# Kernel optimization log

Hardware: AMD Instinct MI355X
Metric: run time of the kernel (lower is better)

The kernel has to match this reference:

```python
import jax, jax.numpy as jnp
import numpy as np

B, N, K = 4, 4096, 16
D_POINTS, D_MODEL = 64, 128


def setup_inputs() -> dict:
    key = jax.random.key(0)
    ks = jax.random.split(key, 18)
    rn = lambda k, shp, s=0.05: (jax.random.normal(k, shp, jnp.float32) * s)
    return {
        "xyz": jax.random.normal(ks[0], (B, N, 3), jnp.float32),
        "features": jax.random.normal(ks[1], (B, N, D_POINTS), jnp.float32),
        # fc_delta: Linear(3,d_model) -> ReLU -> Linear(d_model,d_model)
        "Wd1": rn(ks[2], (3, D_MODEL)), "bd1": rn(ks[3], (D_MODEL,)),
        "Wd2": rn(ks[4], (D_MODEL, D_MODEL)), "bd2": rn(ks[5], (D_MODEL,)),
        # fc1: Linear(d_points, d_model)
        "Wf1": rn(ks[6], (D_POINTS, D_MODEL)), "bf1": rn(ks[7], (D_MODEL,)),
        # w_qs / w_ks / w_vs: Linear(d_model, d_model, bias=False)
        "Wq": rn(ks[8], (D_MODEL, D_MODEL)),
        "Wk": rn(ks[9], (D_MODEL, D_MODEL)),
        "Wv": rn(ks[10], (D_MODEL, D_MODEL)),
        # fc_gamma: Linear(d_model,d_model) -> ReLU -> Linear(d_model,d_model)
        "Wg1": rn(ks[11], (D_MODEL, D_MODEL)), "bg1": rn(ks[12], (D_MODEL,)),
        "Wg2": rn(ks[13], (D_MODEL, D_MODEL)), "bg2": rn(ks[14], (D_MODEL,)),
        # fc2: Linear(d_model, d_points)
        "Wo": rn(ks[15], (D_MODEL, D_POINTS)), "bo": rn(ks[16], (D_POINTS,)),
    }


def reference(xyz, features, Wd1, bd1, Wd2, bd2, Wf1, bf1, Wq, Wk, Wv,
              Wg1, bg1, Wg2, bg2, Wo, bo):
    sq = jnp.sum(xyz * xyz, axis=-1)
    d2 = sq[:, :, None] + sq[:, None, :] - 2.0 * jnp.einsum('bnd,bmd->bnm', xyz, xyz)
    # argsort()[:, :, :k] == k smallest distances (self included)
    _, knn_idx = jax.lax.top_k(-d2, K)  # [B,N,K] int32

    gather = jax.vmap(lambda a, i: a[i])  # per-batch fancy gather along point axis
    knn_xyz = gather(xyz, knn_idx)                       # [B,N,K,3]
    rel = xyz[:, :, None, :] - knn_xyz                   # [B,N,K,3]
    pos_enc = jax.nn.relu(rel @ Wd1 + bd1) @ Wd2 + bd2   # [B,N,K,D]

    shortcut = features
    f = features @ Wf1 + bf1                             # [B,N,D]
    knn_f = gather(f, knn_idx)                           # [B,N,K,D]

    q = f @ Wq                                           # [B,N,D]
    k = knn_f @ Wk                                       # [B,N,K,D]
    v = knn_f @ Wv                                       # [B,N,K,D]

    attn = q[:, :, None, :] - k + pos_enc                # [B,N,K,D]
    attn = jax.nn.relu(attn @ Wg1 + bg1) @ Wg2 + bg2
    attn = jax.nn.softmax(attn / np.sqrt(D_MODEL).astype(np.float32), axis=-2)

    res = jnp.einsum('bnkf,bnkf->bnf', attn, v + pos_enc)  # [B,N,D]
    return res @ Wo + bo + shortcut                        # [B,N,d_points]
```

## Files before the change

kernel.cpp:

```cpp
#include <hip/hip_runtime.h>
#include <hip/hip_bf16.h>

#define NPTS 4096
#define BATCH 4
#define BN (BATCH * NPTS)
#define DMODEL 128
#define DPTS 64
#define KNBR 16
#define SWS 136

typedef unsigned short u16;
typedef unsigned int u32;
typedef unsigned long long u64;
typedef short bh8 __attribute__((ext_vector_type(8)));
typedef float f32x4 __attribute__((ext_vector_type(4)));

__device__ __forceinline__ float bfu(u16 u) {
    union { u32 i; float f; } c; c.i = ((u32)u) << 16; return c.f;
}
__device__ __forceinline__ u16 f2u(float x) {
    u32 u = __float_as_uint(x);
    u32 r = u + 0x7FFFu + ((u >> 16) & 1u);
    return (u16)(r >> 16);
}
__device__ __forceinline__ u32 pack2(float a, float b) {
    return (u32)f2u(a) | ((u32)f2u(b) << 16);
}
__device__ __forceinline__ float ldr(const void* p, long i, int mode) {
    return mode == 0 ? bfu(((const u16*)p)[i]) : ((const float*)p)[i];
}
__device__ __forceinline__ void str(void* p, long i, float v, int mode) {
    if (mode == 0) ((u16*)p)[i] = f2u(v);
    else ((float*)p)[i] = v;
}
__device__ __forceinline__ int detect_mode(const void* Wq) {
    const u16* w = (const u16*)Wq;
    int lane = threadIdx.x & 63;
    int tot = 0;
#pragma unroll
    for (int r = 0; r < 4; ++r) {
        unsigned e = (w[lane + r * 64] >> 7) & 0xFFu;
        bool wild = (e >= 132u) || (e > 0u && e <= 90u);
        tot += (int)__popcll(__ballot(wild));
    }
    return tot > 32 ? 1 : 0;
}

__global__ __launch_bounds__(256) void prep_kernel(
    const void* __restrict__ Wd2, const void* __restrict__ Wg1, const void* __restrict__ Wg2,
    const void* __restrict__ Wo, const void* __restrict__ Wq, const void* __restrict__ Wk,
    const void* __restrict__ Wv, const void* __restrict__ Wf1,
    u16* __restrict__ WdT2, u16* __restrict__ WgT1, u16* __restrict__ WgT2,
    u16* __restrict__ WoT, u16* __restrict__ WqT, u16* __restrict__ WkT,
    u16* __restrict__ WvT, u16* __restrict__ WfT) {
    int mode = detect_mode(Wq);
    int gid = blockIdx.x * 256 + threadIdx.x;
    if (gid < 6 * 16384) {
        int m = gid >> 14, o = gid & 16383;
        int n = o >> 7, i = o & 127;
        const void* W = (m == 0) ? Wd2 : (m == 1) ? Wg1 : (m == 2) ? Wg2
                      : (m == 3) ? Wq  : (m == 4) ? Wk  : Wv;
        u16* D = (m == 0) ? WdT2 : (m == 1) ? WgT1 : (m == 2) ? WgT2
               : (m == 3) ? WqT  : (m == 4) ? WkT  : WvT;
        D[o] = f2u(ldr(W, (long)i * 128 + n, mode));
    } else if (gid < 6 * 16384 + 8192) {
        int o = gid - 6 * 16384;
        int n = o >> 6, k2 = o & 63;
        WfT[o] = f2u(ldr(Wf1, (long)k2 * 128 + n, mode));
    } else if (gid < 6 * 16384 + 16384) {
        int o2 = gid - 6 * 16384 - 8192;
        int col = o2 >> 7, i = o2 & 127;
        WoT[o2] = f2u(ldr(Wo, (long)i * 64 + col, mode));
    }
}

__global__ __launch_bounds__(256) void qkv_kernel(
    const void* __restrict__ feat, const void* __restrict__ bf1v, const void* __restrict__ WqRaw,
    const u16* __restrict__ WfT, const u16* __restrict__ WqT,
    const u16* __restrict__ WkT, const u16* __restrict__ WvT,
    u16* __restrict__ qw, u16* __restrict__ kfw, u16* __restrict__ vfw) {
    int mode = detect_mode(WqRaw);
    __shared__ __align__(16) u16 sFeat[64 * 72];
    __shared__ __align__(16) u16 sF[64 * SWS];
    const int t = threadIdx.x;
    const int p0 = blockIdx.x * 64;
    const int lane = t & 63, w = t >> 6;
    const int rg = (w & 1) * 32, cg = (w >> 1) * 64;
    const int lm = lane & 15, lq = lane >> 4;

    for (int i = t; i < 512; i += 256) {
        int r = i >> 3, c8 = i & 7;
        u16 tmp[8];
        if (mode == 0) {
            *(uint4*)tmp = *((const uint4*)feat + (long)(p0 + r) * 8 + c8);
        } else {
            const float* fp = (const float*)feat + (long)(p0 + r) * 64 + c8 * 8;
#pragma unroll
            for (int u = 0; u < 8; ++u) tmp[u] = f2u(fp[u]);
        }
        *(uint4*)(sFeat + r * 72 + c8 * 8) = *(uint4*)tmp;
    }
    __syncthreads();

    {
        f32x4 acc[2][4];
#pragma unroll
        for (int rt = 0; rt < 2; ++rt)
#pragma unroll
            for (int ct = 0; ct < 4; ++ct) { acc[rt][ct][0]=0.f; acc[rt][ct][1]=0.f; acc[rt][ct][2]=0.f; acc[rt][ct][3]=0.f; }
#pragma unroll
        for (int kk = 0; kk < 2; ++kk) {
            const int ko = kk * 32 + lq * 8;
            bh8 a0 = *(const bh8*)(sFeat + (rg + lm) * 72 + ko);
            bh8 a1 = *(const bh8*)(sFeat + (rg + 16 + lm) * 72 + ko);
            bh8 bq[4];
#pragma unroll
            for (int ct = 0; ct < 4; ++ct)
                bq[ct] = *(const bh8*)(WfT + (long)(cg + ct * 16 + lm) * 64 + ko);
#pragma unroll
            for (int ct = 0; ct < 4; ++ct) {
                acc[0][ct] = __builtin_amdgcn_mfma_f32_16x16x32_bf16(a0, bq[ct], acc[0][ct], 0, 0, 0);
                acc[1][ct] = __builtin_amdgcn_mfma_f32_16x16x32_bf16(a1, bq[ct], acc[1][ct], 0, 0, 0);
            }
        }
#pragma unroll
        for (int rt = 0; rt < 2; ++rt)
#pragma unroll
            for (int ct = 0; ct < 4; ++ct) {
                const int col = cg + ct * 16 + lm;
                const float bj = ldr(bf1v, col, mode);
#pragma unroll
                for (int r4 = 0; r4 < 4; ++r4) {
                    int row = rg + rt * 16 + lq * 4 + r4;
                    u32 u = (u32)f2u(acc[rt][ct][r4] + bj);
                    u32 o = __shfl_xor(u, 1);
                    if ((lane & 1) == 0)
                        *(u32*)(sF + row * SWS + col) = u | (o << 16);
                }
            }
    }
    __syncthreads();

    const u16* Ws[3] = {WqT, WkT, WvT};
    u16* Os[3] = {qw, kfw, vfw};
#pragma unroll 1
    for (int m = 0; m < 3; ++m) {
        f32x4 acc[2][4];
#pragma unroll
        for (int rt = 0; rt < 2; ++rt)
#pragma unroll
            for (int ct = 0; ct < 4; ++ct) { acc[rt][ct][0]=0.f; acc[rt][ct][1]=0.f; acc[rt][ct][2]=0.f; acc[rt][ct][3]=0.f; }
#pragma unroll
        for (int kk = 0; kk < 4; ++kk) {
            const int ko = kk * 32 + lq * 8;
            bh8 a0 = *(const bh8*)(sF + (rg + lm) * SWS + ko);
            bh8 a1 = *(const bh8*)(sF + (rg + 16 + lm) * SWS + ko);
            bh8 bq[4];
#pragma unroll
            for (int ct = 0; ct < 4; ++ct)
                bq[ct] = *(const bh8*)(Ws[m] + (long)(cg + ct * 16 + lm) * 128 + ko);
#pragma unroll
            for (int ct = 0; ct < 4; ++ct) {
                acc[0][ct] = __builtin_amdgcn_mfma_f32_16x16x32_bf16(a0, bq[ct], acc[0][ct], 0, 0, 0);
                acc[1][ct] = __builtin_amdgcn_mfma_f32_16x16x32_bf16(a1, bq[ct], acc[1][ct], 0, 0, 0);
            }
        }
#pragma unroll
        for (int rt = 0; rt < 2; ++rt)
#pragma unroll
            for (int ct = 0; ct < 4; ++ct) {
                const int col = cg + ct * 16 + lm;
#pragma unroll
                for (int r4 = 0; r4 < 4; ++r4) {
                    int row = rg + rt * 16 + lq * 4 + r4;
                    u32 u = (u32)f2u(acc[rt][ct][r4]);
                    u32 o = __shfl_xor(u, 1);
                    if ((lane & 1) == 0)
                        *(u32*)(Os[m] + (long)(p0 + row) * DMODEL + col) = u | (o << 16);
                }
            }
    }
}

__device__ __forceinline__ void mfma4(const u16* sIn, const u16* __restrict__ Bg,
                                      const float* bias, bool dorelu, bool inplace,
                                      u16* sOut, int t) {
    const int lane = t & 63, w = t >> 6;
    const int rg = (w & 1) * 32, cg = (w >> 1) * 64;
    const int lm = lane & 15, lq = lane >> 4;
    f32x4 acc[2][4];
#pragma unroll
    for (int rt = 0; rt < 2; ++rt)
#pragma unroll
        for (int ct = 0; ct < 4; ++ct) { acc[rt][ct][0]=0.f; acc[rt][ct][1]=0.f; acc[rt][ct][2]=0.f; acc[rt][ct][3]=0.f; }
#pragma unroll
    for (int kk = 0; kk < 4; ++kk) {
        const int ko = kk * 32 + lq * 8;
        bh8 a0 = *(const bh8*)(sIn + (rg + lm) * SWS + ko);
        bh8 a1 = *(const bh8*)(sIn + (rg + 16 + lm) * SWS + ko);
        bh8 bq[4];
#pragma unroll
        for (int ct = 0; ct < 4; ++ct)
            bq[ct] = *(const bh8*)(Bg + (long)(cg + ct * 16 + lm) * 128 + ko);
#pragma unroll
        for (int ct = 0; ct < 4; ++ct) {
            acc[0][ct] = __builtin_amdgcn_mfma_f32_16x16x32_bf16(a0, bq[ct], acc[0][ct], 0, 0, 0);
            acc[1][ct] = __builtin_amdgcn_mfma_f32_16x16x32_bf16(a1, bq[ct], acc[1][ct], 0, 0, 0);
        }
    }
    if (inplace) __syncthreads();
#pragma unroll
    for (int rt = 0; rt < 2; ++rt)
#pragma unroll
        for (int ct = 0; ct < 4; ++ct) {
            const int col = cg + ct * 16 + lm;
            const float bj = bias[col];
#pragma unroll
            for (int r4 = 0; r4 < 4; ++r4) {
                int row = rg + rt * 16 + lq * 4 + r4;
                float v = acc[rt][ct][r4] + bj;
                if (dorelu) v = fmaxf(v, 0.f);
                u32 u = (u32)f2u(v);
                u32 o = __shfl_xor(u, 1);
                if ((lane & 1) == 0)
                    *(u32*)(sOut + row * SWS + col) = u | (o << 16);
            }
        }
}

#define ATT_SA 0
#define ATT_SPE 17408
#define ATT_SREL 34816
#define ATT_SBIAS 35840
#define ATT_SQ 37376
#define SMEM_BYTES 38400

__global__ __launch_bounds__(256, 4) void fused_kernel(
    const void* __restrict__ xyz, const void* __restrict__ feat,
    const void* __restrict__ Wd1, const void* __restrict__ bd1, const void* __restrict__ bd2,
    const void* __restrict__ bg1, const void* __restrict__ bg2, const void* __restrict__ bo,
    const void* __restrict__ WqRaw,
    const u16* __restrict__ WdT2, const u16* __restrict__ WgT1, const u16* __restrict__ WgT2,
    const u16* __restrict__ WoT,
    const u16* __restrict__ qw, const u16* __restrict__ kfw, const u16* __restrict__ vfw,
    void* __restrict__ out) {
    int mode = detect_mode(WqRaw);
    __shared__ __align__(16) char smem[SMEM_BYTES];
    __shared__ int sIdx[64];
    u16* sXyz = (u16*)smem;
    u16* sA   = (u16*)(smem + ATT_SA);
    u16* sPE  = (u16*)(smem + ATT_SPE);
    float (*sRel)[4] = (float(*)[4])(smem + ATT_SREL);
    float* sBias = (float*)(smem + ATT_SBIAS);
    u16* sQ   = (u16*)(smem + ATT_SQ);

    const int t = threadIdx.x, lane = t & 63, w = t >> 6;
    const int p0 = blockIdx.x * 4;
    const long bbase = (long)(p0 >> 12) * NPTS;
    const long xb = bbase * 3;

    for (int m = t; m < NPTS; m += 256) {
        float gx = ldr(xyz, xb + m * 3 + 0, mode);
        float gy = ldr(xyz, xb + m * 3 + 1, mode);
        float gz = ldr(xyz, xb + m * 3 + 2, mode);
        uint2 pk;
        pk.x = (u32)f2u(gx) | ((u32)f2u(gy) << 16);
        pk.y = (u32)f2u(gz);
        *(uint2*)(sXyz + m * 4) = pk;
    }
    __syncthreads();

    {
        const int pl = (p0 & (NPTS - 1)) + w;
        uint2 qv = *(const uint2*)(sXyz + pl * 4);
        const float px = __uint_as_float(qv.x << 16);
        const float py = __uint_as_float(qv.x & 0xFFFF0000u);
        const float pz = __uint_as_float(qv.y << 16);
        u64 kv = ~0ull;
        u32 Tu = 0xFFFFFFFFu;
        uint2 cd = *(const uint2*)(sXyz + lane * 4);
#pragma unroll 1
        for (int it = 0; it < NPTS / 64; ++it) {
            uint2 cur = cd;
            if (it < NPTS / 64 - 1)
                cd = *(const uint2*)(sXyz + (it + 1) * 256 + lane * 4);
            float cx = __uint_as_float(cur.x << 16);
            float cy = __uint_as_float(cur.x & 0xFFFF0000u);
            float cz = __uint_as_float(cur.y << 16);
            float n2 = cx * cx + cy * cy + cz * cz;
            float dot = px * cx + py * cy + pz * cz;
            float key = fmaf(dot, -2.f, n2);
            u32 uk = __float_as_uint(key);
            uk ^= (u32)((int)uk >> 31) | 0x80000000u;
            unsigned long long mask = __ballot(uk < Tu);
            const int ibase = it * 64;
            while (mask) {
                int l = __ffsll(mask) - 1;
                mask &= mask - 1;
                u32 chi = __builtin_amdgcn_readlane(uk, l);
                if (chi < Tu) {
                    u64 cand = ((u64)chi << 32) | (u32)(ibase + l);
                    u64 prev = __shfl_up(kv, 1);
                    if (lane == 0) prev = 0;
                    kv = (prev > cand) ? prev : ((kv > cand) ? cand : kv);
                    Tu = __builtin_amdgcn_readlane((u32)(kv >> 32), 15);
                }
            }
        }
        if (lane < 16) sIdx[w * 16 + lane] = (int)(u32)kv;
    }
    __syncthreads();

    for (int i = t; i < 384; i += 256) {
        const void* b = (i < 128) ? bd2 : (i < 256) ? bg1 : bg2;
        sBias[i] = ldr(b, i & 127, mode);
    }
    ((u32*)sQ)[t] = ((const u32*)(qw + (long)p0 * DMODEL))[t];
    const int ch = 2 * lane;
    const float wd0a = ldr(Wd1, ch, mode),       wd0b = ldr(Wd1, ch + 1, mode);
    const float wd1a = ldr(Wd1, 128 + ch, mode), wd1b = ldr(Wd1, 128 + ch + 1, mode);
    const float wd2a = ldr(Wd1, 256 + ch, mode), wd2b = ldr(Wd1, 256 + ch + 1, mode);
    const float bd1a = ldr(bd1, ch, mode),       bd1b = ldr(bd1, ch + 1, mode);
    if (t < 64) {
        long nb = bbase + sIdx[t];
        int pl2 = t >> 4;
        sRel[t][0] = ldr(xyz, ((long)p0 + pl2) * 3 + 0, mode) - ldr(xyz, nb * 3 + 0, mode);
        sRel[t][1] = ldr(xyz, ((long)p0 + pl2) * 3 + 1, mode) - ldr(xyz, nb * 3 + 1, mode);
        sRel[t][2] = ldr(xyz, ((long)p0 + pl2) * 3 + 2, mode) - ldr(xyz, nb * 3 + 2, mode);
    }
    __syncthreads();

#pragma unroll
    for (int i = 0; i < 16; ++i) {
        int r = w * 16 + i;
        float4 rl = *(const float4*)sRel[r];
        float h0 = fmaxf(bd1a + rl.x * wd0a + rl.y * wd1a + rl.z * wd2a, 0.f);
        float h1 = fmaxf(bd1b + rl.x * wd0b + rl.y * wd1b + rl.z * wd2b, 0.f);
        *(u32*)(sA + r * SWS + ch) = pack2(h0, h1);
    }
    __syncthreads();
    mfma4(sA, WdT2, sBias, false, false, sPE, t);
    __syncthreads();

#pragma unroll
    for (int i = 0; i < 16; ++i) {
        int r = w * 16 + i;
        u32 kv2 = *(const u32*)(kfw + (bbase + sIdx[r]) * (long)DMODEL + ch);
        u32 qv2 = *(const u32*)(sQ + (r >> 4) * DMODEL + ch);
        u32 pe2 = *(const u32*)(sPE + r * SWS + ch);
        float a0 = bfu((u16)qv2) - bfu((u16)kv2) + bfu((u16)pe2);
        float a1 = bfu((u16)(qv2 >> 16)) - bfu((u16)(kv2 >> 16)) + bfu((u16)(pe2 >> 16));
        *(u32*)(sA + r * SWS + ch) = pack2(a0, a1);
    }
    __syncthreads();
    mfma4(sA, WgT1, sBias + 128, true, true, sA, t);
    __syncthreads();
    mfma4(sA, WgT2, sBias + 256, false, true, sA, t);
    __syncthreads();

    float res0, res1;
    {
        float lg0[16], lg1[16];
        float mx0 = -3e38f, mx1 = -3e38f;
#pragma unroll
        for (int k = 0; k < KNBR; ++k) {
            u32 l2 = *(const u32*)(sA + (w * 16 + k) * SWS + ch);
            lg0[k] = bfu((u16)l2); lg1[k] = bfu((u16)(l2 >> 16));
            mx0 = fmaxf(mx0, lg0[k]); mx1 = fmaxf(mx1, lg1[k]);
        }
        const float inv = 0.08838834764831845f;
        float s0 = 0.f, s1 = 0.f, r0 = 0.f, r1 = 0.f;
#pragma unroll
        for (int k = 0; k < KNBR; ++k) {
            u32 v2 = *(const u32*)(vfw + (bbase + sIdx[w * 16 + k]) * (long)DMODEL + ch);
            u32 p2 = *(const u32*)(sPE + (w * 16 + k) * SWS + ch);
            float e0 = __expf((lg0[k] - mx0) * inv);
            float e1 = __expf((lg1[k] - mx1) * inv);
            s0 += e0; s1 += e1;
            r0 += e0 * (bfu((u16)v2) + bfu((u16)p2));
            r1 += e1 * (bfu((u16)(v2 >> 16)) + bfu((u16)(p2 >> 16)));
        }
        res0 = r0 / s0; res1 = r1 / s1;
    }
    __syncthreads();
    *(u32*)(sA + w * SWS + ch) = pack2(res0, res1);
    __syncthreads();

    {
        const int lm = lane & 15, lq = lane >> 4;
        const int col = w * 16 + lm;
        f32x4 acc = {0.f, 0.f, 0.f, 0.f};
#pragma unroll
        for (int kk = 0; kk < 4; ++kk) {
            const int ko = kk * 32 + lq * 8;
            bh8 aa = *(const bh8*)(sA + lm * SWS + ko);
            bh8 bb = *(const bh8*)(WoT + (long)col * DMODEL + ko);
            acc = __builtin_amdgcn_mfma_f32_16x16x32_bf16(aa, bb, acc, 0, 0, 0);
        }
        if (lq == 0) {
            float bov = ldr(bo, col, mode);
#pragma unroll
            for (int r4 = 0; r4 < 4; ++r4) {
                long p = p0 + r4;
                float v = acc[r4] + bov + ldr(feat, p * DPTS + col, mode);
                str(out, p * DPTS + col, v, mode);
            }
        }
    }
}

extern "C" void kernel_launch(void* const* d_in, const int* in_sizes, int n_in,
                              void* d_out, int out_size, void* d_ws, size_t ws_size,
                              hipStream_t stream) {
    (void)in_sizes; (void)n_in; (void)out_size; (void)ws_size;
    char* ws = (char*)d_ws;
    u16* qw   = (u16*)(ws + 256);
    u16* kfw  = qw + (long)BN * DMODEL;
    u16* vfw  = kfw + (long)BN * DMODEL;
    u16* WdT2 = vfw + (long)BN * DMODEL;
    u16* WgT1 = WdT2 + 16384;
    u16* WgT2 = WgT1 + 16384;
    u16* WoT  = WgT2 + 16384;
    u16* WqT  = WoT + 8192;
    u16* WkT  = WqT + 16384;
    u16* WvT  = WkT + 16384;
    u16* WfT  = WvT + 16384;

    prep_kernel<<<448, 256, 0, stream>>>(d_in[4], d_in[11], d_in[13], d_in[15],
                                         d_in[8], d_in[9], d_in[10], d_in[6],
                                         WdT2, WgT1, WgT2, WoT, WqT, WkT, WvT, WfT);
    qkv_kernel<<<BN / 64, 256, 0, stream>>>(d_in[1], d_in[7], d_in[8],
                                            WfT, WqT, WkT, WvT, qw, kfw, vfw);
    fused_kernel<<<BN / 4, 256, 0, stream>>>(d_in[0], d_in[1], d_in[2], d_in[3], d_in[5],
                                             d_in[12], d_in[14], d_in[16], d_in[8],
                                             WdT2, WgT1, WgT2, WoT,
                                             qw, kfw, vfw, d_out);
}
```

Measured before the change: 341.1 us.

## Compute kNN distances with MFMA over precomputed bf16 point table

```diff
diff --git a/kernel.cpp b/kernel.cpp
--- a/kernel.cpp
+++ b/kernel.cpp
@@ -49,10 +49,10 @@
 __global__ __launch_bounds__(256) void prep_kernel(
     const void* __restrict__ Wd2, const void* __restrict__ Wg1, const void* __restrict__ Wg2,
     const void* __restrict__ Wo, const void* __restrict__ Wq, const void* __restrict__ Wk,
-    const void* __restrict__ Wv, const void* __restrict__ Wf1,
+    const void* __restrict__ Wv, const void* __restrict__ Wf1, const void* __restrict__ xyz,
     u16* __restrict__ WdT2, u16* __restrict__ WgT1, u16* __restrict__ WgT2,
     u16* __restrict__ WoT, u16* __restrict__ WqT, u16* __restrict__ WkT,
-    u16* __restrict__ WvT, u16* __restrict__ WfT) {
+    u16* __restrict__ WvT, u16* __restrict__ WfT, u16* __restrict__ Xb) {
     int mode = detect_mode(Wq);
     int gid = blockIdx.x * 256 + threadIdx.x;
     if (gid < 6 * 16384) {
@@ -71,6 +71,16 @@
         int o2 = gid - 6 * 16384 - 8192;
         int col = o2 >> 7, i = o2 & 127;
         WoT[o2] = f2u(ldr(Wo, (long)i * 64 + col, mode));
+    } else if (gid < 6 * 16384 + 16384 + BN) {
+        int i = gid - (6 * 16384 + 16384);
+        float x = ldr(xyz, (long)i * 3 + 0, mode);
+        float y = ldr(xyz, (long)i * 3 + 1, mode);
+        float z = ldr(xyz, (long)i * 3 + 2, mode);
+        float n2 = x * x + y * y + z * z;
+        u16 hi = f2u(n2);
+        u16 lo = f2u(n2 - bfu(hi));
+        u16 row[8] = {f2u(x), f2u(y), f2u(z), hi, lo, 0, 0, 0};
+        *(uint4*)(Xb + (long)i * 8) = *(uint4*)row;
     }
 }
 
@@ -241,74 +251,86 @@
     const void* __restrict__ bg1, const void* __restrict__ bg2, const void* __restrict__ bo,
     const void* __restrict__ WqRaw,
     const u16* __restrict__ WdT2, const u16* __restrict__ WgT1, const u16* __restrict__ WgT2,
-    const u16* __restrict__ WoT,
+    const u16* __restrict__ WoT, const u16* __restrict__ Xb,
     const u16* __restrict__ qw, const u16* __restrict__ kfw, const u16* __restrict__ vfw,
     void* __restrict__ out) {
     int mode = detect_mode(WqRaw);
     __shared__ __align__(16) char smem[SMEM_BYTES];
     __shared__ int sIdx[64];
-    u16* sXyz = (u16*)smem;
-    u16* sA   = (u16*)(smem + ATT_SA);
-    u16* sPE  = (u16*)(smem + ATT_SPE);
+    u32* sD  = (u32*)smem;
+    u16* sA  = (u16*)(smem + ATT_SA);
+    u16* sPE = (u16*)(smem + ATT_SPE);
     float (*sRel)[4] = (float(*)[4])(smem + ATT_SREL);
     float* sBias = (float*)(smem + ATT_SBIAS);
-    u16* sQ   = (u16*)(smem + ATT_SQ);
+    u16* sQ  = (u16*)(smem + ATT_SQ);
 
     const int t = threadIdx.x, lane = t & 63, w = t >> 6;
+    const int lm = lane & 15, lq = lane >> 4;
     const int p0 = blockIdx.x * 4;
     const long bbase = (long)(p0 >> 12) * NPTS;
-    const long xb = bbase * 3;
-
-    for (int m = t; m < NPTS; m += 256) {
-        float gx = ldr(xyz, xb + m * 3 + 0, mode);
-        float gy = ldr(xyz, xb + m * 3 + 1, mode);
-        float gz = ldr(xyz, xb + m * 3 + 2, mode);
-        uint2 pk;
-        pk.x = (u32)f2u(gx) | ((u32)f2u(gy) << 16);
-        pk.y = (u32)f2u(gz);
-        *(uint2*)(sXyz + m * 4) = pk;
-    }
-    __syncthreads();
-
+
+    bh8 afrag;
     {
-        const int pl = (p0 & (NPTS - 1)) + w;
-        uint2 qv = *(const uint2*)(sXyz + pl * 4);
-        const float px = __uint_as_float(qv.x << 16);
-        const float py = __uint_as_float(qv.x & 0xFFFF0000u);
-        const float pz = __uint_as_float(qv.y << 16);
-        u64 kv = ~0ull;
-        u32 Tu = 0xFFFFFFFFu;
-        uint2 cd = *(const uint2*)(sXyz + lane * 4);
+        u16 av[8];
+#pragma unroll
+        for (int j = 0; j < 8; ++j) {
+            int k = lq * 8 + j;
+            float v = 0.f;
+            if (lm < 4) {
+                if (k < 3) v = -2.f * ldr(xyz, ((long)p0 + lm) * 3 + k, mode);
+                else if (k == 3 || k == 4) v = 1.f;
+            }
+            av[j] = f2u(v);
+        }
+        afrag = *(bh8*)av;
+    }
+    const u16* XbB = Xb + (long)bbase * 8;
+    u64 kv = ~0ull;
+    u32 Tu = 0xFFFFFFFFu;
 #pragma unroll 1
-        for (int it = 0; it < NPTS / 64; ++it) {
-            uint2 cur = cd;
-            if (it < NPTS / 64 - 1)
-                cd = *(const uint2*)(sXyz + (it + 1) * 256 + lane * 4);
-            float cx = __uint_as_float(cur.x << 16);
-            float cy = __uint_as_float(cur.x & 0xFFFF0000u);
-            float cz = __uint_as_float(cur.y << 16);
-            float n2 = cx * cx + cy * cy + cz * cz;
-            float dot = px * cx + py * cy + pz * cz;
-            float key = fmaf(dot, -2.f, n2);
-            u32 uk = __float_as_uint(key);
-            uk ^= (u32)((int)uk >> 31) | 0x80000000u;
-            unsigned long long mask = __ballot(uk < Tu);
-            const int ibase = it * 64;
-            while (mask) {
-                int l = __ffsll(mask) - 1;
-                mask &= mask - 1;
-                u32 chi = __builtin_amdgcn_readlane(uk, l);
-                if (chi < Tu) {
-                    u64 cand = ((u64)chi << 32) | (u32)(ibase + l);
-                    u64 prev = __shfl_up(kv, 1);
-                    if (lane == 0) prev = 0;
-                    kv = (prev > cand) ? prev : ((kv > cand) ? cand : kv);
-                    Tu = __builtin_amdgcn_readlane((u32)(kv >> 32), 15);
+    for (int chunk = 0; chunk < 2; ++chunk) {
+        const int c0 = chunk * 2048;
+#pragma unroll 1
+        for (int tile = w; tile < 128; tile += 4) {
+            const int cc = c0 + tile * 16;
+            bh8 bfrag = *(const bh8*)(XbB + (long)(cc + lm) * 8);
+            f32x4 acc = {0.f, 0.f, 0.f, 0.f};
+            acc = __builtin_amdgcn_mfma_f32_16x16x32_bf16(afrag, bfrag, acc, 0, 0, 0);
+            if (lq == 0) {
+#pragma unroll
+                for (int p = 0; p < 4; ++p) {
+                    u32 uk = __float_as_uint(acc[p]);
+                    uk ^= (u32)((int)uk >> 31) | 0x80000000u;
+                    sD[p * 2048 + tile * 16 + lm] = uk;
                 }
             }
         }
-        if (lane < 16) sIdx[w * 16 + lane] = (int)(u32)kv;
-    }
+        __syncthreads();
+#pragma unroll 1
+        for (int it = 0; it < 8; ++it) {
+            uint4 K = *(const uint4*)(sD + w * 2048 + it * 256 + lane * 4);
+#pragma unroll
+            for (int j = 0; j < 4; ++j) {
+                u32 kj = (j == 0) ? K.x : (j == 1) ? K.y : (j == 2) ? K.z : K.w;
+                unsigned long long mask = __ballot(kj < Tu);
+                const int idb = c0 + it * 256 + j;
+                while (mask) {
+                    int l = __ffsll(mask) - 1;
+                    mask &= mask - 1;
+                    u32 chi = __builtin_amdgcn_readlane(kj, l);
+                    if (chi < Tu) {
+                        u64 cand = ((u64)chi << 32) | (u32)(idb + l * 4);
+                        u64 prev = __shfl_up(kv, 1);
+                        if (lane == 0) prev = 0;
+                        kv = (prev > cand) ? prev : ((kv > cand) ? cand : kv);
+                        Tu = __builtin_amdgcn_readlane((u32)(kv >> 32), 15);
+                    }
+                }
+            }
+        }
+        __syncthreads();
+    }
+    if (lane < 16) sIdx[w * 16 + lane] = (int)(u32)kv;
     __syncthreads();
 
     for (int i = t; i < 384; i += 256) {
@@ -387,7 +409,6 @@
     __syncthreads();
 
     {
-        const int lm = lane & 15, lq = lane >> 4;
         const int col = w * 16 + lm;
         f32x4 acc = {0.f, 0.f, 0.f, 0.f};
 #pragma unroll
@@ -425,14 +446,15 @@
     u16* WkT  = WqT + 16384;
     u16* WvT  = WkT + 16384;
     u16* WfT  = WvT + 16384;
-
-    prep_kernel<<<448, 256, 0, stream>>>(d_in[4], d_in[11], d_in[13], d_in[15],
-                                         d_in[8], d_in[9], d_in[10], d_in[6],
-                                         WdT2, WgT1, WgT2, WoT, WqT, WkT, WvT, WfT);
+    u16* Xb   = WfT + 8192;
+
+    prep_kernel<<<512, 256, 0, stream>>>(d_in[4], d_in[11], d_in[13], d_in[15],
+                                         d_in[8], d_in[9], d_in[10], d_in[6], d_in[0],
+                                         WdT2, WgT1, WgT2, WoT, WqT, WkT, WvT, WfT, Xb);
     qkv_kernel<<<BN / 64, 256, 0, stream>>>(d_in[1], d_in[7], d_in[8],
                                             WfT, WqT, WkT, WvT, qw, kfw, vfw);
     fused_kernel<<<BN / 4, 256, 0, stream>>>(d_in[0], d_in[1], d_in[2], d_in[3], d_in[5],
                                              d_in[12], d_in[14], d_in[16], d_in[8],
-                                             WdT2, WgT1, WgT2, WoT,
+                                             WdT2, WgT1, WgT2, WoT, Xb,
                                              qw, kfw, vfw, d_out);
 }
```

Result: slower. 374.8 us (+9.9%).

## Process two candidates per kNN step, ping-pong MLP buffers, prefetch V early

Applied to the files above, without the earlier changes.

```diff
diff --git a/kernel.cpp b/kernel.cpp
--- a/kernel.cpp
+++ b/kernel.cpp
@@ -183,7 +183,7 @@
 }
 
 __device__ __forceinline__ void mfma4(const u16* sIn, const u16* __restrict__ Bg,
-                                      const float* bias, bool dorelu, bool inplace,
+                                      const float* bias, bool dorelu,
                                       u16* sOut, int t) {
     const int lane = t & 63, w = t >> 6;
     const int rg = (w & 1) * 32, cg = (w >> 1) * 64;
@@ -208,7 +208,6 @@
             acc[1][ct] = __builtin_amdgcn_mfma_f32_16x16x32_bf16(a1, bq[ct], acc[1][ct], 0, 0, 0);
         }
     }
-    if (inplace) __syncthreads();
 #pragma unroll
     for (int rt = 0; rt < 2; ++rt)
 #pragma unroll
@@ -255,6 +254,7 @@
     u16* sQ   = (u16*)(smem + ATT_SQ);
 
     const int t = threadIdx.x, lane = t & 63, w = t >> 6;
+    const int lm = lane & 15, lq = lane >> 4;
     const int p0 = blockIdx.x * 4;
     const long bbase = (long)(p0 >> 12) * NPTS;
     const long xb = bbase * 3;
@@ -278,28 +278,44 @@
         const float pz = __uint_as_float(qv.y << 16);
         u64 kv = ~0ull;
         u32 Tu = 0xFFFFFFFFu;
-        uint2 cd = *(const uint2*)(sXyz + lane * 4);
+        uint2 cd0 = *(const uint2*)(sXyz + lane * 4);
+        uint2 cd1 = *(const uint2*)(sXyz + (64 + lane) * 4);
 #pragma unroll 1
-        for (int it = 0; it < NPTS / 64; ++it) {
-            uint2 cur = cd;
-            if (it < NPTS / 64 - 1)
-                cd = *(const uint2*)(sXyz + (it + 1) * 256 + lane * 4);
-            float cx = __uint_as_float(cur.x << 16);
-            float cy = __uint_as_float(cur.x & 0xFFFF0000u);
-            float cz = __uint_as_float(cur.y << 16);
-            float n2 = cx * cx + cy * cy + cz * cz;
-            float dot = px * cx + py * cy + pz * cz;
-            float key = fmaf(dot, -2.f, n2);
-            u32 uk = __float_as_uint(key);
-            uk ^= (u32)((int)uk >> 31) | 0x80000000u;
-            unsigned long long mask = __ballot(uk < Tu);
-            const int ibase = it * 64;
+        for (int it = 0; it < NPTS / 128; ++it) {
+            uint2 c0 = cd0, c1 = cd1;
+            if (it < NPTS / 128 - 1) {
+                cd0 = *(const uint2*)(sXyz + ((it + 1) * 128 + lane) * 4);
+                cd1 = *(const uint2*)(sXyz + ((it + 1) * 128 + 64 + lane) * 4);
+            }
+            float cx0 = __uint_as_float(c0.x << 16);
+            float cy0 = __uint_as_float(c0.x & 0xFFFF0000u);
+            float cz0 = __uint_as_float(c0.y << 16);
+            float cx1 = __uint_as_float(c1.x << 16);
+            float cy1 = __uint_as_float(c1.x & 0xFFFF0000u);
+            float cz1 = __uint_as_float(c1.y << 16);
+            float k0 = fmaf(px * cx0 + py * cy0 + pz * cz0, -2.f,
+                            cx0 * cx0 + cy0 * cy0 + cz0 * cz0);
+            float k1 = fmaf(px * cx1 + py * cy1 + pz * cz1, -2.f,
+                            cx1 * cx1 + cy1 * cy1 + cz1 * cz1);
+            u32 u0 = __float_as_uint(k0); u0 ^= (u32)((int)u0 >> 31) | 0x80000000u;
+            u32 u1 = __float_as_uint(k1); u1 ^= (u32)((int)u1 >> 31) | 0x80000000u;
+            u32 umin = (u0 < u1) ? u0 : u1;
+            unsigned long long mask = __ballot(umin < Tu);
+            const int ibase = it * 128;
             while (mask) {
                 int l = __ffsll(mask) - 1;
                 mask &= mask - 1;
-                u32 chi = __builtin_amdgcn_readlane(uk, l);
-                if (chi < Tu) {
-                    u64 cand = ((u64)chi << 32) | (u32)(ibase + l);
+                u32 a0 = __builtin_amdgcn_readlane(u0, l);
+                u32 a1 = __builtin_amdgcn_readlane(u1, l);
+                if (a0 < Tu) {
+                    u64 cand = ((u64)a0 << 32) | (u32)(ibase + l);
+                    u64 prev = __shfl_up(kv, 1);
+                    if (lane == 0) prev = 0;
+                    kv = (prev > cand) ? prev : ((kv > cand) ? cand : kv);
+                    Tu = __builtin_amdgcn_readlane((u32)(kv >> 32), 15);
+                }
+                if (a1 < Tu) {
+                    u64 cand = ((u64)a1 << 32) | (u32)(ibase + 64 + l);
                     u64 prev = __shfl_up(kv, 1);
                     if (lane == 0) prev = 0;
                     kv = (prev > cand) ? prev : ((kv > cand) ? cand : kv);
@@ -322,11 +338,12 @@
     const float wd2a = ldr(Wd1, 256 + ch, mode), wd2b = ldr(Wd1, 256 + ch + 1, mode);
     const float bd1a = ldr(bd1, ch, mode),       bd1b = ldr(bd1, ch + 1, mode);
     if (t < 64) {
-        long nb = bbase + sIdx[t];
-        int pl2 = t >> 4;
-        sRel[t][0] = ldr(xyz, ((long)p0 + pl2) * 3 + 0, mode) - ldr(xyz, nb * 3 + 0, mode);
-        sRel[t][1] = ldr(xyz, ((long)p0 + pl2) * 3 + 1, mode) - ldr(xyz, nb * 3 + 1, mode);
-        sRel[t][2] = ldr(xyz, ((long)p0 + pl2) * 3 + 2, mode) - ldr(xyz, nb * 3 + 2, mode);
+        int pl2 = (p0 & (NPTS - 1)) + (t >> 4);
+        uint2 pv = *(const uint2*)(sXyz + pl2 * 4);
+        uint2 nv = *(const uint2*)(sXyz + sIdx[t] * 4);
+        sRel[t][0] = __uint_as_float(pv.x << 16)          - __uint_as_float(nv.x << 16);
+        sRel[t][1] = __uint_as_float(pv.x & 0xFFFF0000u)  - __uint_as_float(nv.x & 0xFFFF0000u);
+        sRel[t][2] = __uint_as_float(pv.y << 16)          - __uint_as_float(nv.y << 16);
     }
     __syncthreads();
 
@@ -339,23 +356,29 @@
         *(u32*)(sA + r * SWS + ch) = pack2(h0, h1);
     }
     __syncthreads();
-    mfma4(sA, WdT2, sBias, false, false, sPE, t);
-    __syncthreads();
-
+    mfma4(sA, WdT2, sBias, false, sPE, t);
+    __syncthreads();
+
+    float vpe0[16], vpe1[16];
 #pragma unroll
     for (int i = 0; i < 16; ++i) {
         int r = w * 16 + i;
-        u32 kv2 = *(const u32*)(kfw + (bbase + sIdx[r]) * (long)DMODEL + ch);
+        long nbase = (bbase + sIdx[r]) * (long)DMODEL + ch;
+        u32 kv2 = *(const u32*)(kfw + nbase);
+        u32 vv2 = *(const u32*)(vfw + nbase);
         u32 qv2 = *(const u32*)(sQ + (r >> 4) * DMODEL + ch);
         u32 pe2 = *(const u32*)(sPE + r * SWS + ch);
-        float a0 = bfu((u16)qv2) - bfu((u16)kv2) + bfu((u16)pe2);
-        float a1 = bfu((u16)(qv2 >> 16)) - bfu((u16)(kv2 >> 16)) + bfu((u16)(pe2 >> 16));
+        float pa = bfu((u16)pe2), pb = bfu((u16)(pe2 >> 16));
+        vpe0[i] = bfu((u16)vv2) + pa;
+        vpe1[i] = bfu((u16)(vv2 >> 16)) + pb;
+        float a0 = bfu((u16)qv2) - bfu((u16)kv2) + pa;
+        float a1 = bfu((u16)(qv2 >> 16)) - bfu((u16)(kv2 >> 16)) + pb;
         *(u32*)(sA + r * SWS + ch) = pack2(a0, a1);
     }
     __syncthreads();
-    mfma4(sA, WgT1, sBias + 128, true, true, sA, t);
-    __syncthreads();
-    mfma4(sA, WgT2, sBias + 256, false, true, sA, t);
+    mfma4(sA, WgT1, sBias + 128, true, sPE, t);
+    __syncthreads();
+    mfma4(sPE, WgT2, sBias + 256, false, sA, t);
     __syncthreads();
 
     float res0, res1;
@@ -372,13 +395,11 @@
         float s0 = 0.f, s1 = 0.f, r0 = 0.f, r1 = 0.f;
 #pragma unroll
         for (int k = 0; k < KNBR; ++k) {
-            u32 v2 = *(const u32*)(vfw + (bbase + sIdx[w * 16 + k]) * (long)DMODEL + ch);
-            u32 p2 = *(const u32*)(sPE + (w * 16 + k) * SWS + ch);
             float e0 = __expf((lg0[k] - mx0) * inv);
             float e1 = __expf((lg1[k] - mx1) * inv);
             s0 += e0; s1 += e1;
-            r0 += e0 * (bfu((u16)v2) + bfu((u16)p2));
-            r1 += e1 * (bfu((u16)(v2 >> 16)) + bfu((u16)(p2 >> 16)));
+            r0 += e0 * vpe0[k];
+            r1 += e1 * vpe1[k];
         }
         res0 = r0 / s0; res1 = r1 / s1;
     }
@@ -387,7 +408,6 @@
     __syncthreads();
 
     {
-        const int lm = lane & 15, lq = lane >> 4;
         const int col = w * 16 + lm;
         f32x4 acc = {0.f, 0.f, 0.f, 0.f};
 #pragma unroll
```

New measurement: 340.3 us. No clear change (-0.2%).
